# Performance work log

Measured on AMD Instinct MI355X. Metric: run time of the kernel, lower is better.

## Reference

```python
import jax, jax.numpy as jnp
import numpy as np

NUM_HEADS = 16
D_IN = 1024
D_OUT = 64  # = D_IN // NUM_HEADS
N = 2048


def setup_inputs() -> dict:
    key = jax.random.key(0)
    kx, kq, kk, kv, ko = jax.random.split(key, 5)
    x = jax.random.normal(kx, (N, D_IN), dtype=jnp.float32)
    # per-head projection weights, stacked over heads (torch code keeps a
    # Python list of SelfAttention modules; stacking is the vectorized form)
    q_proj = jax.random.normal(kq, (NUM_HEADS, D_IN, D_OUT), dtype=jnp.float32)
    k_proj = jax.random.normal(kk, (NUM_HEADS, D_IN, D_OUT), dtype=jnp.float32)
    v_proj = jax.random.normal(kv, (NUM_HEADS, D_IN, D_OUT), dtype=jnp.float32)
    o_proj = jax.random.normal(ko, (D_IN, D_IN), dtype=jnp.float32)
    return {"x": x, "q_proj": q_proj, "k_proj": k_proj, "v_proj": v_proj, "o_proj": o_proj}


def reference(x, q_proj, k_proj, v_proj, o_proj):
    d_out = q_proj.shape[-1]
    # per-head projections: [H, N, E]
    q = jnp.einsum('nd,hde->hne', x, q_proj)
    k = jnp.einsum('nd,hde->hne', x, k_proj)
    v = jnp.einsum('nd,hde->hne', x, v_proj)
    # full NxN scores per head (matches the naive torch implementation's math)
    scores = jnp.einsum('hne,hme->hnm', q, k) / jnp.sqrt(jnp.float32(d_out))
    attn = jax.nn.softmax(scores, axis=-1)
    ctx = jnp.einsum('hnm,hme->hne', attn, v)
    # concat heads along the feature dim (head 0 first, as in torch.cat)
    h, n, e = ctx.shape
    out = jnp.transpose(ctx, (1, 0, 2)).reshape(n, h * e)
    return out @ o_proj
```

## Files before the change

kernel.cpp:

```cpp
#include <hip/hip_runtime.h>

#define H 16
#define N 2048
#define E 64
#define D 1024

typedef __attribute__((ext_vector_type(8))) short bf16x8;
typedef __attribute__((ext_vector_type(4))) float f32x4;
typedef __attribute__((ext_vector_type(4))) unsigned int u32x4;

__device__ __forceinline__ float bf2f(unsigned short u) {
    union { unsigned int i; float f; } v;
    v.i = ((unsigned int)u) << 16;
    return v.f;
}
__device__ __forceinline__ unsigned short f2bf(float f) {
    unsigned int u = __float_as_uint(f);
    return (unsigned short)((u + 0x7fffu + ((u >> 16) & 1u)) >> 16);
}
__device__ __forceinline__ unsigned int cvtpk(float lo, float hi) {
    unsigned int r;
    asm("v_cvt_pk_bf16_f32 %0, %1, %2" : "=v"(r) : "v"(lo), "v"(hi));
    return r;
}
__device__ __forceinline__ bf16x8 pk4(unsigned int a, unsigned int b,
                                      unsigned int c, unsigned int d) {
    union { u32x4 u; bf16x8 h; } x;
    x.u = (u32x4){a, b, c, d};
    return x.h;
}
__device__ __forceinline__ float ex2(float x) {
    float r;
    asm("v_exp_f32 %0, %1" : "=v"(r) : "v"(x));
    return r;
}
#define MFMA(a, b, c) __builtin_amdgcn_mfma_f32_16x16x32_bf16(a, b, c, 0, 0, 0)

typedef __attribute__((address_space(3))) unsigned int lds_u32;
typedef const __attribute__((address_space(1))) unsigned int glb_u32;
__device__ __forceinline__ void dma16(const unsigned short* g, unsigned short* l) {
    __builtin_amdgcn_global_load_lds((glb_u32*)g, (lds_u32*)l, 16, 0, 0);
}

__device__ __forceinline__ int sw8(int row, int c)  { return row * 64  + ((c ^ (row & 7)) << 3); }
__device__ __forceinline__ int sw16(int row, int c) { return row * 128 + ((c ^ (row & 7)) << 3); }

__global__ __launch_bounds__(256) void convert_all_kernel(
    const float* __restrict__ x,
    const float* __restrict__ qw, const float* __restrict__ kw,
    const float* __restrict__ vw, const float* __restrict__ ow,
    unsigned short* __restrict__ xh, unsigned short* __restrict__ xl,
    unsigned short* __restrict__ wBh, unsigned short* __restrict__ wBl,
    unsigned short* __restrict__ wvt, unsigned short* __restrict__ woh)
{
    __shared__ float ts[64][65];
    const int b0 = blockIdx.x;
    const int t = threadIdx.x;
    if (b0 < 2048) {
        const int i = (b0 * 256 + t) * 4;
        const float4 v = *(const float4*)&x[i];
        ushort4 hh, ll;
        hh.x = f2bf(v.x); ll.x = f2bf(v.x - bf2f(hh.x));
        hh.y = f2bf(v.y); ll.y = f2bf(v.y - bf2f(hh.y));
        hh.z = f2bf(v.z); ll.z = f2bf(v.z - bf2f(hh.z));
        hh.w = f2bf(v.w); ll.w = f2bf(v.w - bf2f(hh.w));
        *(ushort4*)&xh[i] = hh;
        *(ushort4*)&xl[i] = ll;
        return;
    }
    const int b = b0 - 2048;
    const float* src;
    int rs, dt, orow0;
    bool has_lo;
    unsigned short *dh, *dl;
    if (b < 768) {
        const int which = b >> 8, r = b & 255, h = r >> 4;
        dt = r & 15;
        src = (which == 0 ? qw : which == 1 ? kw : vw) + ((size_t)h * D + dt * 64) * E;
        rs = E;
        if (which == 0)      { dh = wBh; dl = wBl; orow0 = h * 64;        has_lo = true; }
        else if (which == 1) { dh = wBh; dl = wBl; orow0 = 1024 + h * 64; has_lo = true; }
        else                 { dh = wvt; dl = wBl; orow0 = h * 64;        has_lo = false; }
    } else {
        const int r = b - 768, ct = r >> 4;
        dt = r & 15;
        src = ow + (size_t)(dt * 64) * D + ct * 64;
        rs = D;
        orow0 = ct * 64;
        dh = woh; dl = wBl; has_lo = false;
    }
    {
        const int row = t >> 2, cb = (t & 3) * 16;
        #pragma unroll
        for (int j = 0; j < 16; j += 4) {
            const float4 v = *(const float4*)&src[row * rs + cb + j];
            ts[row][cb + j + 0] = v.x;
            ts[row][cb + j + 1] = v.y;
            ts[row][cb + j + 2] = v.z;
            ts[row][cb + j + 3] = v.w;
        }
    }
    __syncthreads();
    {
        const int cl = t >> 2, dp = (t & 3) * 16;
        bf16x8 hv0, hv1, lv0, lv1;
        #pragma unroll
        for (int i = 0; i < 16; ++i) {
            const float f = ts[dp + i][cl];
            const unsigned short hh = f2bf(f);
            const unsigned short lo = f2bf(f - bf2f(hh));
            if (i < 8) { hv0[i] = (short)hh; lv0[i] = (short)lo; }
            else       { hv1[i - 8] = (short)hh; lv1[i - 8] = (short)lo; }
        }
        const size_t o = (size_t)(orow0 + cl) * D + dt * 64 + dp;
        *(bf16x8*)&dh[o] = hv0;
        *(bf16x8*)&dh[o + 8] = hv1;
        if (has_lo) {
            *(bf16x8*)&dl[o] = lv0;
            *(bf16x8*)&dl[o + 8] = lv1;
        }
    }
}

__global__ __launch_bounds__(256, 3) void qkv_kernel(
    const unsigned short* __restrict__ xh, const unsigned short* __restrict__ xl,
    const unsigned short* __restrict__ wBh, const unsigned short* __restrict__ wBl,
    const unsigned short* __restrict__ wvt,
    unsigned short* __restrict__ Qh, unsigned short* __restrict__ Ql,
    unsigned short* __restrict__ Kh, unsigned short* __restrict__ Kl,
    unsigned short* __restrict__ Vt)
{
    __shared__ unsigned short ash[128 * 64], asl[128 * 64];
    __shared__ unsigned short bsh[64 * 64], bsl[64 * 64];
    const int n0 = blockIdx.x * 128;
    const int ct0 = blockIdx.y;
    const int sec = ct0 >> 4;
    const int hh = ct0 & 15;
    const bool isv = (sec == 2);
    const unsigned short* Bh = isv ? wvt : wBh;
    const size_t brow0 = (sec == 1 ? 1024 : 0) + hh * 64;

    const int t = threadIdx.x;
    const int lane = t & 63, wvi = t >> 6, quad = lane >> 4, l15 = lane & 15;

    f32x4 acc[2][4];
    #pragma unroll
    for (int i = 0; i < 2; ++i)
        #pragma unroll
        for (int j = 0; j < 4; ++j) acc[i][j] = (f32x4){0.f, 0.f, 0.f, 0.f};

    for (int k0 = 0; k0 < D; k0 += 64) {
        __syncthreads();
        #pragma unroll
        for (int p = 0; p < 4; ++p) {
            const int row = p * 32 + wvi * 8 + (lane >> 3);
            const int lc = (lane & 7) ^ (row & 7);
            const int lo = p * 2048 + wvi * 512 + lane * 8;
            const size_t ga = (size_t)(n0 + row) * D + k0 + lc * 8;
            dma16(&xh[ga], &ash[lo]);
            if (!isv) dma16(&xl[ga], &asl[lo]);
        }
        #pragma unroll
        for (int p = 0; p < 2; ++p) {
            const int row = p * 32 + wvi * 8 + (lane >> 3);
            const int lc = (lane & 7) ^ (row & 7);
            const int lo = p * 2048 + wvi * 512 + lane * 8;
            const size_t gb = (brow0 + row) * D + k0 + lc * 8;
            dma16(&Bh[gb], &bsh[lo]);
            if (!isv) dma16(&wBl[gb], &bsl[lo]);
        }
        __syncthreads();

        #pragma unroll
        for (int kwi = 0; kwi < 2; ++kwi) {
            const int c = kwi * 4 + quad;
            bf16x8 ah[2], al[2], bh[4], bl[4];
            #pragma unroll
            for (int i = 0; i < 2; ++i) {
                ah[i] = *(const bf16x8*)&ash[sw8(wvi * 32 + i * 16 + l15, c)];
                if (!isv) al[i] = *(const bf16x8*)&asl[sw8(wvi * 32 + i * 16 + l15, c)];
            }
            #pragma unroll
            for (int j = 0; j < 4; ++j) {
                bh[j] = *(const bf16x8*)&bsh[sw8(j * 16 + l15, c)];
                if (!isv) bl[j] = *(const bf16x8*)&bsl[sw8(j * 16 + l15, c)];
            }
            #pragma unroll
            for (int i = 0; i < 2; ++i)
                #pragma unroll
                for (int j = 0; j < 4; ++j) {
                    acc[i][j] = MFMA(ah[i], bh[j], acc[i][j]);
                    if (!isv) {
                        acc[i][j] = MFMA(ah[i], bl[j], acc[i][j]);
                        acc[i][j] = MFMA(al[i], bh[j], acc[i][j]);
                    }
                }
        }
    }

    if (isv) {
        #pragma unroll
        for (int j = 0; j < 4; ++j) {
            const int e = j * 16 + l15;
            #pragma unroll
            for (int i = 0; i < 2; ++i) {
                const int nb = n0 + wvi * 32 + i * 16 + quad * 4;
                ushort4 pk;
                pk.x = f2bf(acc[i][j][0]);
                pk.y = f2bf(acc[i][j][1]);
                pk.z = f2bf(acc[i][j][2]);
                pk.w = f2bf(acc[i][j][3]);
                *(ushort4*)&Vt[((size_t)hh * 64 + e) * N + nb] = pk;
            }
        }
    } else {
        const float scale = (sec == 0) ? 0.18033688011112042f : 1.0f;
        unsigned short* Oh = (sec == 0) ? Qh : Kh;
        unsigned short* Ol = (sec == 0) ? Ql : Kl;
        #pragma unroll
        for (int j = 0; j < 4; ++j) {
            const int e = j * 16 + l15;
            #pragma unroll
            for (int i = 0; i < 2; ++i)
                #pragma unroll
                for (int r = 0; r < 4; ++r) {
                    const int n = n0 + wvi * 32 + i * 16 + quad * 4 + r;
                    const float val = acc[i][j][r] * scale;
                    const unsigned short hv = f2bf(val);
                    Oh[((size_t)hh * N + n) * E + e] = hv;
                    Ol[((size_t)hh * N + n) * E + e] = f2bf(val - bf2f(hv));
                }
        }
    }
}

__global__ __launch_bounds__(256, 2) void attn_kernel(
    const unsigned short* __restrict__ Qh, const unsigned short* __restrict__ Ql,
    const unsigned short* __restrict__ Kh, const unsigned short* __restrict__ Kl,
    const unsigned short* __restrict__ Vt,
    unsigned short* __restrict__ Op0, unsigned short* __restrict__ Op1,
    float* __restrict__ mlp)
{
    __shared__ unsigned short kbuf[2 * 16384];
    __shared__ unsigned short vts[64 * 128];
    const int r0 = blockIdx.x * 128, h = blockIdx.y, split = blockIdx.z;
    const int mb = split * 1024;
    const int t = threadIdx.x, lane = t & 63, wvi = t >> 6, quad = lane >> 4, l15 = lane & 15;

    bf16x8 qfh[2][2], qfl[2][2];
    #pragma unroll
    for (int i = 0; i < 2; ++i) {
        const size_t base = ((size_t)h * N + r0 + wvi * 32 + i * 16 + l15) * E;
        #pragma unroll
        for (int kwi = 0; kwi < 2; ++kwi) {
            qfh[i][kwi] = *(const bf16x8*)&Qh[base + kwi * 32 + quad * 8];
            qfl[i][kwi] = *(const bf16x8*)&Ql[base + kwi * 32 + quad * 8];
        }
    }

    f32x4 oacc[2][4];
    float mrow[2] = {-1e30f, -1e30f}, lrow[2] = {0.f, 0.f};
    #pragma unroll
    for (int i = 0; i < 2; ++i)
        #pragma unroll
        for (int j = 0; j < 4; ++j) oacc[i][j] = (f32x4){0.f, 0.f, 0.f, 0.f};

    const int ve = wvi * 16 + (lane >> 2);
    const int vc = lane & 3;

    #pragma unroll
    for (int p = 0; p < 4; ++p) {
        const int row = p * 32 + wvi * 8 + (lane >> 3);
        const int lc = (lane & 7) ^ (row & 7);
        const int lo = p * 2048 + wvi * 512 + lane * 8;
        const size_t gk = ((size_t)h * N + mb + row) * E + lc * 8;
        dma16(&Kh[gk], &kbuf[lo]);
        dma16(&Kl[gk], &kbuf[8192 + lo]);
    }

    for (int it = 0; it < 8; ++it) {
        const int cur = it & 1;
        __syncthreads();
        const int mcol = mb + it * 128;

        uint2 vr0[4], vr1[4];
        #pragma unroll
        for (int z = 0; z < 4; ++z) {
            const size_t gb = ((size_t)h * 64 + ve) * N + mcol + vc * 32 + z * 4;
            vr0[z] = *(const uint2*)&Vt[gb];
            vr1[z] = *(const uint2*)&Vt[gb + 16];
        }

        const unsigned short* ksh = &kbuf[cur * 16384];
        const unsigned short* ksl = ksh + 8192;

        f32x4 s[2][8];
        #pragma unroll
        for (int i = 0; i < 2; ++i)
            #pragma unroll
            for (int ct = 0; ct < 8; ++ct) s[i][ct] = (f32x4){0.f, 0.f, 0.f, 0.f};

        __builtin_amdgcn_s_setprio(1);
        #pragma unroll
        for (int kwi = 0; kwi < 2; ++kwi) {
            const int c = kwi * 4 + quad;
            #pragma unroll
            for (int ct = 0; ct < 8; ++ct) {
                const bf16x8 kh = *(const bf16x8*)&ksh[sw8(ct * 16 + l15, c)];
                const bf16x8 kl = *(const bf16x8*)&ksl[sw8(ct * 16 + l15, c)];
                #pragma unroll
                for (int i = 0; i < 2; ++i) {
                    s[i][ct] = MFMA(kh, qfh[i][kwi], s[i][ct]);
                    s[i][ct] = MFMA(kl, qfh[i][kwi], s[i][ct]);
                    s[i][ct] = MFMA(kh, qfl[i][kwi], s[i][ct]);
                }
            }
        }
        __builtin_amdgcn_s_setprio(0);

        #pragma unroll
        for (int i = 0; i < 2; ++i) {
            float m0 = s[i][0][0], m1 = s[i][0][1], m2 = s[i][0][2], m3 = s[i][0][3];
            #pragma unroll
            for (int ct = 1; ct < 8; ++ct) {
                m0 = fmaxf(m0, s[i][ct][0]); m1 = fmaxf(m1, s[i][ct][1]);
                m2 = fmaxf(m2, s[i][ct][2]); m3 = fmaxf(m3, s[i][ct][3]);
            }
            float mx = fmaxf(fmaxf(m0, m1), fmaxf(m2, m3));
            mx = fmaxf(mx, __shfl_xor(mx, 16));
            mx = fmaxf(mx, __shfl_xor(mx, 32));
            if (__any(mx > mrow[i])) {
                const float mn = fmaxf(mrow[i], mx);
                const float al = ex2(mrow[i] - mn);
                mrow[i] = mn;
                lrow[i] *= al;
                #pragma unroll
                for (int ct = 0; ct < 4; ++ct) {
                    oacc[i][ct][0] *= al; oacc[i][ct][1] *= al;
                    oacc[i][ct][2] *= al; oacc[i][ct][3] *= al;
                }
            }
            const float mn = mrow[i];
            float s0 = 0.f, s1 = 0.f, s2 = 0.f, s3 = 0.f;
            #pragma unroll
            for (int ct = 0; ct < 8; ++ct) {
                const float p0 = ex2(s[i][ct][0] - mn);
                const float p1 = ex2(s[i][ct][1] - mn);
                const float p2 = ex2(s[i][ct][2] - mn);
                const float p3 = ex2(s[i][ct][3] - mn);
                s[i][ct][0] = p0; s[i][ct][1] = p1;
                s[i][ct][2] = p2; s[i][ct][3] = p3;
                s0 += p0; s1 += p1; s2 += p2; s3 += p3;
            }
            float sum = (s0 + s1) + (s2 + s3);
            sum += __shfl_xor(sum, 16);
            sum += __shfl_xor(sum, 32);
            lrow[i] += sum;
        }

        #pragma unroll
        for (int z = 0; z < 4; ++z) {
            const int c16 = vc * 4 + z;
            u32x4 w = (u32x4){vr0[z].x, vr0[z].y, vr1[z].x, vr1[z].y};
            *(u32x4*)&vts[ve * 128 + ((c16 ^ (ve & 7)) << 3)] = w;
        }
        __syncthreads();

        if (it < 7) {
            #pragma unroll
            for (int p = 0; p < 4; ++p) {
                const int row = p * 32 + wvi * 8 + (lane >> 3);
                const int lc = (lane & 7) ^ (row & 7);
                const int lo = (cur ^ 1) * 16384 + p * 2048 + wvi * 512 + lane * 8;
                const size_t gk = ((size_t)h * N + mcol + 128 + row) * E + lc * 8;
                dma16(&Kh[gk], &kbuf[lo]);
                dma16(&Kl[gk], &kbuf[8192 + lo]);
            }
        }

        #pragma unroll
        for (int kb = 0; kb < 4; ++kb) {
            bf16x8 pb[2];
            #pragma unroll
            for (int i = 0; i < 2; ++i)
                pb[i] = pk4(cvtpk(s[i][2 * kb][0],     s[i][2 * kb][1]),
                            cvtpk(s[i][2 * kb][2],     s[i][2 * kb][3]),
                            cvtpk(s[i][2 * kb + 1][0], s[i][2 * kb + 1][1]),
                            cvtpk(s[i][2 * kb + 1][2], s[i][2 * kb + 1][3]));
            __builtin_amdgcn_s_setprio(1);
            #pragma unroll
            for (int ct = 0; ct < 4; ++ct) {
                const int re = ct * 16 + l15;
                const bf16x8 va =
                    *(const bf16x8*)&vts[re * 128 + (((kb * 4 + quad) ^ (re & 7)) << 3)];
                #pragma unroll
                for (int i = 0; i < 2; ++i)
                    oacc[i][ct] = MFMA(va, pb[i], oacc[i][ct]);
            }
            __builtin_amdgcn_s_setprio(0);
        }
    }

    unsigned short* Opc = split ? Op1 : Op0;
    #pragma unroll
    for (int i = 0; i < 2; ++i) {
        const int n = r0 + wvi * 32 + i * 16 + l15;
        if (quad == 0) {
            mlp[(((size_t)split * 16 + h) * 2048 + n) * 2 + 0] = mrow[i];
            mlp[(((size_t)split * 16 + h) * 2048 + n) * 2 + 1] = lrow[i];
        }
        #pragma unroll
        for (int ct = 0; ct < 4; ++ct) {
            ushort4 pk;
            pk.x = f2bf(oacc[i][ct][0]);
            pk.y = f2bf(oacc[i][ct][1]);
            pk.z = f2bf(oacc[i][ct][2]);
            pk.w = f2bf(oacc[i][ct][3]);
            *(ushort4*)&Opc[((size_t)h * 2048 + n) * 64 + ct * 16 + quad * 4] = pk;
        }
    }
}

__global__ __launch_bounds__(256) void combine_kernel(
    const unsigned short* __restrict__ Op0, const unsigned short* __restrict__ Op1,
    const float* __restrict__ mlp, unsigned short* __restrict__ Ch)
{
    const int h = blockIdx.y;
    const int n = blockIdx.x * 64 + (threadIdx.x >> 2);
    const int e0 = (threadIdx.x & 3) * 16;
    const float m0 = mlp[((size_t)h * 2048 + n) * 2 + 0];
    const float l0 = mlp[((size_t)h * 2048 + n) * 2 + 1];
    const float m1 = mlp[((size_t)(16 + h) * 2048 + n) * 2 + 0];
    const float l1 = mlp[((size_t)(16 + h) * 2048 + n) * 2 + 1];
    const float M = fmaxf(m0, m1);
    const float a0 = ex2(m0 - M), a1 = ex2(m1 - M);
    const float inv = 1.f / (l0 * a0 + l1 * a1);
    const size_t ib = ((size_t)h * 2048 + n) * 64 + e0;
    const size_t ob = (size_t)n * D + h * 64 + e0;
    #pragma unroll
    for (int j = 0; j < 2; ++j) {
        const bf16x8 v0 = *(const bf16x8*)&Op0[ib + j * 8];
        const bf16x8 v1 = *(const bf16x8*)&Op1[ib + j * 8];
        bf16x8 o;
        #pragma unroll
        for (int k = 0; k < 8; ++k) {
            const float c = (bf2f((unsigned short)v0[k]) * a0 +
                             bf2f((unsigned short)v1[k]) * a1) * inv;
            o[k] = (short)f2bf(c);
        }
        *(bf16x8*)&Ch[ob + j * 8] = o;
    }
}

__global__ __launch_bounds__(256, 4) void out_proj_kernel(
    const unsigned short* __restrict__ Chh, const unsigned short* __restrict__ Wh,
    float* __restrict__ out)
{
    __shared__ unsigned short ash[64 * 128], bsh[64 * 128];
    const int n0 = blockIdx.x * 64, c0 = blockIdx.y * 64;
    const int t = threadIdx.x, lane = t & 63, wvi = t >> 6, quad = lane >> 4, l15 = lane & 15;

    f32x4 acc[4];
    #pragma unroll
    for (int j = 0; j < 4; ++j) acc[j] = (f32x4){0.f, 0.f, 0.f, 0.f};

    for (int k0 = 0; k0 < D; k0 += 128) {
        __syncthreads();
        #pragma unroll
        for (int p = 0; p < 4; ++p) {
            const int row = p * 16 + wvi * 4 + quad;
            const int lc = l15 ^ (row & 7);
            const int lo = p * 2048 + wvi * 512 + lane * 8;
            dma16(&Chh[(size_t)(n0 + row) * D + k0 + lc * 8], &ash[lo]);
            dma16(&Wh[(size_t)(c0 + row) * D + k0 + lc * 8], &bsh[lo]);
        }
        __syncthreads();

        #pragma unroll
        for (int kwi = 0; kwi < 4; ++kwi) {
            const int c = kwi * 4 + quad;
            const bf16x8 ah = *(const bf16x8*)&ash[sw16(wvi * 16 + l15, c)];
            #pragma unroll
            for (int j = 0; j < 4; ++j) {
                const bf16x8 bh = *(const bf16x8*)&bsh[sw16(j * 16 + l15, c)];
                acc[j] = MFMA(ah, bh, acc[j]);
            }
        }
    }

    #pragma unroll
    for (int r = 0; r < 4; ++r) {
        const int n = n0 + wvi * 16 + quad * 4 + r;
        #pragma unroll
        for (int j = 0; j < 4; ++j)
            out[(size_t)n * D + c0 + j * 16 + l15] = acc[j][r];
    }
}

extern "C" void kernel_launch(void* const* d_in, const int* in_sizes, int n_in,
                              void* d_out, int out_size, void* d_ws, size_t ws_size,
                              hipStream_t stream) {
    const float* x  = (const float*)d_in[0];
    const float* qw = (const float*)d_in[1];
    const float* kw = (const float*)d_in[2];
    const float* vw = (const float*)d_in[3];
    const float* ow = (const float*)d_in[4];
    float* out = (float*)d_out;

    unsigned short* ws = (unsigned short*)d_ws;
    const size_t M1 = 1024 * 1024;
    unsigned short* wBh = ws;
    unsigned short* wBl = ws + 2 * M1;
    unsigned short* wvt = ws + 4 * M1;
    unsigned short* woh = ws + 5 * M1;
    unsigned short* xh  = ws + 6 * M1;
    unsigned short* xl  = ws + 8 * M1;
    unsigned short* Qh  = ws + 10 * M1;
    unsigned short* Ql  = ws + 12 * M1;
    unsigned short* Kh  = ws + 14 * M1;
    unsigned short* Kl  = ws + 16 * M1;
    unsigned short* Vt  = ws + 18 * M1;
    unsigned short* Ch  = xh;

    unsigned short* Op0 = wBh;
    unsigned short* Op1 = wBl;
    float* mlp = (float*)wvt;

    convert_all_kernel<<<3072, 256, 0, stream>>>(x, qw, kw, vw, ow,
                                                 xh, xl, wBh, wBl, wvt, woh);
    qkv_kernel<<<dim3(16, 48), 256, 0, stream>>>(xh, xl, wBh, wBl, wvt,
                                                 Qh, Ql, Kh, Kl, Vt);
    attn_kernel<<<dim3(16, 16, 2), 256, 0, stream>>>(Qh, Ql, Kh, Kl, Vt,
                                                     Op0, Op1, mlp);
    combine_kernel<<<dim3(32, 16), 256, 0, stream>>>(Op0, Op1, mlp, Ch);
    out_proj_kernel<<<dim3(32, 16), 256, 0, stream>>>(Ch, woh, out);
}
```

Baseline: 160.3 us.

## Split attention keys three ways with single K buffer for higher occupancy

The key dimension is now split into three uneven chunks (6, 5 and 5 tiles of 128 keys) instead of two halves. This gives 768 attention blocks, and the launch bound rises to 3 blocks per CU. To fit three blocks in LDS, the K tile buffer goes from double to single, so the next K tile load now overlaps only with the PV stage. The combine kernel merges three partial outputs using their max and sum statistics, and the third partial output reuses the freed xl workspace. The risks are register pressure or spills under the tighter launch bound, less load/compute overlap, and extra combine traffic.

```diff
diff --git a/kernel.cpp b/kernel.cpp
--- a/kernel.cpp
+++ b/kernel.cpp
@@ -234,17 +234,18 @@
     }
 }
 
-__global__ __launch_bounds__(256, 2) void attn_kernel(
+__global__ __launch_bounds__(256, 3) void attn_kernel(
     const unsigned short* __restrict__ Qh, const unsigned short* __restrict__ Ql,
     const unsigned short* __restrict__ Kh, const unsigned short* __restrict__ Kl,
     const unsigned short* __restrict__ Vt,
     unsigned short* __restrict__ Op0, unsigned short* __restrict__ Op1,
-    float* __restrict__ mlp)
+    unsigned short* __restrict__ Op2, float* __restrict__ mlp)
 {
-    __shared__ unsigned short kbuf[2 * 16384];
+    __shared__ unsigned short kbuf[16384];
     __shared__ unsigned short vts[64 * 128];
     const int r0 = blockIdx.x * 128, h = blockIdx.y, split = blockIdx.z;
-    const int mb = split * 1024;
+    const int mb = split * 640 + (split ? 128 : 0);
+    const int iters = split ? 5 : 6;
     const int t = threadIdx.x, lane = t & 63, wvi = t >> 6, quad = lane >> 4, l15 = lane & 15;
 
     bf16x8 qfh[2][2], qfl[2][2];
@@ -278,8 +279,7 @@
         dma16(&Kl[gk], &kbuf[8192 + lo]);
     }
 
-    for (int it = 0; it < 8; ++it) {
-        const int cur = it & 1;
+    for (int it = 0; it < iters; ++it) {
         __syncthreads();
         const int mcol = mb + it * 128;
 
@@ -291,8 +291,8 @@
             vr1[z] = *(const uint2*)&Vt[gb + 16];
         }
 
-        const unsigned short* ksh = &kbuf[cur * 16384];
-        const unsigned short* ksl = ksh + 8192;
+        const unsigned short* ksh = kbuf;
+        const unsigned short* ksl = kbuf + 8192;
 
         f32x4 s[2][8];
         #pragma unroll
@@ -366,12 +366,12 @@
         }
         __syncthreads();
 
-        if (it < 7) {
+        if (it < iters - 1) {
             #pragma unroll
             for (int p = 0; p < 4; ++p) {
                 const int row = p * 32 + wvi * 8 + (lane >> 3);
                 const int lc = (lane & 7) ^ (row & 7);
-                const int lo = (cur ^ 1) * 16384 + p * 2048 + wvi * 512 + lane * 8;
+                const int lo = p * 2048 + wvi * 512 + lane * 8;
                 const size_t gk = ((size_t)h * N + mcol + 128 + row) * E + lc * 8;
                 dma16(&Kh[gk], &kbuf[lo]);
                 dma16(&Kl[gk], &kbuf[8192 + lo]);
@@ -401,7 +401,7 @@
         }
     }
 
-    unsigned short* Opc = split ? Op1 : Op0;
+    unsigned short* Opc = (split == 0) ? Op0 : (split == 1) ? Op1 : Op2;
     #pragma unroll
     for (int i = 0; i < 2; ++i) {
         const int n = r0 + wvi * 32 + i * 16 + l15;
@@ -423,6 +423,7 @@
 
 __global__ __launch_bounds__(256) void combine_kernel(
     const unsigned short* __restrict__ Op0, const unsigned short* __restrict__ Op1,
+    const unsigned short* __restrict__ Op2,
     const float* __restrict__ mlp, unsigned short* __restrict__ Ch)
 {
     const int h = blockIdx.y;
@@ -432,20 +433,24 @@
     const float l0 = mlp[((size_t)h * 2048 + n) * 2 + 1];
     const float m1 = mlp[((size_t)(16 + h) * 2048 + n) * 2 + 0];
     const float l1 = mlp[((size_t)(16 + h) * 2048 + n) * 2 + 1];
-    const float M = fmaxf(m0, m1);
-    const float a0 = ex2(m0 - M), a1 = ex2(m1 - M);
-    const float inv = 1.f / (l0 * a0 + l1 * a1);
+    const float m2 = mlp[((size_t)(32 + h) * 2048 + n) * 2 + 0];
+    const float l2 = mlp[((size_t)(32 + h) * 2048 + n) * 2 + 1];
+    const float M = fmaxf(fmaxf(m0, m1), m2);
+    const float a0 = ex2(m0 - M), a1 = ex2(m1 - M), a2 = ex2(m2 - M);
+    const float inv = 1.f / (l0 * a0 + l1 * a1 + l2 * a2);
     const size_t ib = ((size_t)h * 2048 + n) * 64 + e0;
     const size_t ob = (size_t)n * D + h * 64 + e0;
     #pragma unroll
     for (int j = 0; j < 2; ++j) {
         const bf16x8 v0 = *(const bf16x8*)&Op0[ib + j * 8];
         const bf16x8 v1 = *(const bf16x8*)&Op1[ib + j * 8];
+        const bf16x8 v2 = *(const bf16x8*)&Op2[ib + j * 8];
         bf16x8 o;
         #pragma unroll
         for (int k = 0; k < 8; ++k) {
             const float c = (bf2f((unsigned short)v0[k]) * a0 +
-                             bf2f((unsigned short)v1[k]) * a1) * inv;
+                             bf2f((unsigned short)v1[k]) * a1 +
+                             bf2f((unsigned short)v2[k]) * a2) * inv;
             o[k] = (short)f2bf(c);
         }
         *(bf16x8*)&Ch[ob + j * 8] = o;
@@ -524,14 +529,15 @@
 
     unsigned short* Op0 = wBh;
     unsigned short* Op1 = wBl;
+    unsigned short* Op2 = xl;
     float* mlp = (float*)wvt;
 
     convert_all_kernel<<<3072, 256, 0, stream>>>(x, qw, kw, vw, ow,
                                                  xh, xl, wBh, wBl, wvt, woh);
     qkv_kernel<<<dim3(16, 48), 256, 0, stream>>>(xh, xl, wBh, wBl, wvt,
                                                  Qh, Ql, Kh, Kl, Vt);
-    attn_kernel<<<dim3(16, 16, 2), 256, 0, stream>>>(Qh, Ql, Kh, Kl, Vt,
-                                                     Op0, Op1, mlp);
-    combine_kernel<<<dim3(32, 16), 256, 0, stream>>>(Op0, Op1, mlp, Ch);
+    attn_kernel<<<dim3(16, 16, 3), 256, 0, stream>>>(Qh, Ql, Kh, Kl, Vt,
+                                                     Op0, Op1, Op2, mlp);
+    combine_kernel<<<dim3(32, 16), 256, 0, stream>>>(Op0, Op1, Op2, mlp, Ch);
     out_proj_kernel<<<dim3(32, 16), 256, 0, stream>>>(Ch, woh, out);
 }
```

New measurement: 176.5 us. +10.1%, slower.
